# Performance work log

Measured on AMD Instinct MI355X. Metric: run time of the kernel, lower is better.

## Reference

```python
import jax, jax.numpy as jnp
import numpy as np
import math

B, S, H = 2, 2048, 2048
NH, HD, SLOTS = 16, 128, 16


def setup_inputs() -> dict:
    key = jax.random.key(0)
    k1, k2, k3, k4 = jax.random.split(key, 4)
    return {
        "hidden_states": jax.random.normal(k1, (B, S, H), dtype=jnp.float32),
        "stack": jax.random.normal(k2, (B, S, NH, SLOTS, HD), dtype=jnp.float32),
        "mask": jnp.ones((B, S, NH, SLOTS), dtype=jnp.float32),
        "W_action": jax.random.normal(k3, (3 * NH, H), dtype=jnp.float32) * 0.02,
        "b_action": jnp.zeros((3 * NH,), dtype=jnp.float32),
        "W_gate": jax.random.normal(k4, (1, HD), dtype=jnp.float32) * 0.02,
        "b_gate": jnp.zeros((1,), dtype=jnp.float32),
        "res_weight": jnp.ones((1,), dtype=jnp.float32),
    }


def reference(hidden_states, stack, mask, W_action, b_action, W_gate, b_gate, res_weight):
    b, s, h = hidden_states.shape
    nh, slots, hd = stack.shape[2], stack.shape[3], stack.shape[4]

    # action probabilities: push / pop / no-op per head
    logits = (jnp.einsum('bsh,ah->bsa', hidden_states, W_action) + b_action) / math.sqrt(hd)
    actions = jax.nn.softmax(logits.reshape(b, s, nh, 3), axis=-1)  # [B,S,NH,3]

    k_values = hidden_states.reshape(b, s, nh, hd)

    # shifted stack views (slot axis = 3)
    push_stack = jnp.concatenate([k_values[:, :, :, None, :], stack[:, :, :, :-1, :]], axis=3)
    push_mask = jnp.concatenate([jnp.ones_like(mask[:, :, :, :1]), mask[:, :, :, :-1]], axis=3)
    pop_stack = jnp.concatenate([stack[:, :, :, 1:, :], jnp.zeros_like(stack[:, :, :, :1, :])], axis=3)
    pop_mask = jnp.concatenate([mask[:, :, :, 1:], jnp.zeros_like(mask[:, :, :, :1])], axis=3)

    a_push = actions[:, :, :, 0]
    a_pop = actions[:, :, :, 1]
    a_stay = actions[:, :, :, 2]

    new_stack = (a_push[..., None, None] * push_stack
                 + a_pop[..., None, None] * pop_stack
                 + a_stay[..., None, None] * stack)  # [B,S,NH,SLOTS,HD]
    new_mask = (a_push[..., None] * push_mask
                + a_pop[..., None] * pop_mask
                + a_stay[..., None] * mask)  # [B,S,NH,SLOTS]

    # gated readout over slots
    gate_scores = jnp.einsum('bsnkd,d->bsnk', new_stack, W_gate[0]) + b_gate[0]
    gate_weights = jax.nn.softmax(gate_scores + (1.0 - new_mask) * -1e9, axis=-1)
    memory_output = jnp.einsum('bsnkd,bsnk->bsnd', new_stack, gate_weights).reshape(b, s, h)

    output = memory_output * res_weight + hidden_states
    return output, new_stack, new_mask
```

## Files before the change

kernel.cpp:

```cpp
#include <hip/hip_runtime.h>

#define Bc 2
#define Sc 2048
#define Hc 2048
#define NHc 16
#define HDc 128
#define SLOTSc 16

__global__ __launch_bounds__(512, 4) void stack_mem_fused(
    const float* __restrict__ hidden,
    const float* __restrict__ stack,
    const float* __restrict__ mask,
    const float* __restrict__ W_action,
    const float* __restrict__ b_action,
    const float* __restrict__ W_gate,
    const float* __restrict__ b_gate,
    const float* __restrict__ res_weight,
    float* __restrict__ out,
    float* __restrict__ new_stack,
    float* __restrict__ new_mask)
{
    __shared__ float hid[Hc];

    const int bs   = blockIdx.x >> 1;
    const int half = blockIdx.x & 1;
    const int tid  = threadIdx.x;
    const int lane = tid & 63;
    const int wave = tid >> 6;
    const int n    = half * 8 + wave;

    const float* hrow = hidden + (size_t)bs * Hc;
    ((float4*)hid)[tid] = ((const float4*)hrow)[tid];
    __syncthreads();

    float p0 = 0.f, p1 = 0.f, p2 = 0.f;
    {
        const float* W0 = W_action + (size_t)(3 * n) * Hc;
        const float* W1 = W0 + Hc;
        const float* W2 = W1 + Hc;
        #pragma unroll 4
        for (int i = lane; i < Hc; i += 64) {
            float hv = hid[i];
            p0 = fmaf(hv, W0[i], p0);
            p1 = fmaf(hv, W1[i], p1);
            p2 = fmaf(hv, W2[i], p2);
        }
    }
    #pragma unroll
    for (int o = 32; o; o >>= 1) {
        p0 += __shfl_xor(p0, o, 64);
        p1 += __shfl_xor(p1, o, 64);
        p2 += __shfl_xor(p2, o, 64);
    }
    const float scale = 0.08838834764831845f;
    float l0 = (p0 + b_action[3 * n + 0]) * scale;
    float l1 = (p1 + b_action[3 * n + 1]) * scale;
    float l2 = (p2 + b_action[3 * n + 2]) * scale;
    float lm = fmaxf(l0, fmaxf(l1, l2));
    float e0 = __expf(l0 - lm), e1 = __expf(l1 - lm), e2 = __expf(l2 - lm);
    float inv3 = 1.f / (e0 + e1 + e2);
    const float a_push = e0 * inv3;
    const float a_pop  = e1 * inv3;
    const float a_stay = e2 * inv3;

    const size_t sbase = ((size_t)bs * NHc + n) * (size_t)(SLOTSc * HDc);
    const float2* st2  = (const float2*)(stack + sbase);
    float2*       nst2 = (float2*)(new_stack + sbase);

    float2 kv = *(const float2*)(hid + n * HDc + 2 * lane);
    float2 wg = *(const float2*)(W_gate + 2 * lane);
    const float bg = b_gate[0];
    const float rw = res_weight[0];

    const float* mp = mask + ((size_t)bs * NHc + n) * SLOTSc;
    float m[SLOTSc];
    {
        float4 q0 = ((const float4*)mp)[0];
        float4 q1 = ((const float4*)mp)[1];
        float4 q2 = ((const float4*)mp)[2];
        float4 q3 = ((const float4*)mp)[3];
        m[0]=q0.x;  m[1]=q0.y;  m[2]=q0.z;  m[3]=q0.w;
        m[4]=q1.x;  m[5]=q1.y;  m[6]=q1.z;  m[7]=q1.w;
        m[8]=q2.x;  m[9]=q2.y;  m[10]=q2.z; m[11]=q2.w;
        m[12]=q3.x; m[13]=q3.y; m[14]=q3.z; m[15]=q3.w;
    }

    float nm[SLOTSc];
    #pragma unroll
    for (int k = 0; k < SLOTSc; ++k) {
        float pm = (k == 0) ? 1.f : m[k - 1];
        float om = (k < SLOTSc - 1) ? m[k + 1] : 0.f;
        nm[k] = a_push * pm + a_pop * om + a_stay * m[k];
    }
    {
        float msel = nm[0];
        #pragma unroll
        for (int k = 1; k < SLOTSc; ++k) if (lane == k) msel = nm[k];
        if (lane < SLOTSc)
            new_mask[((size_t)bs * NHc + n) * SLOTSc + lane] = msel;
    }
    float bias[SLOTSc];
    #pragma unroll
    for (int k = 0; k < SLOTSc; ++k)
        bias[k] = bg + (1.f - nm[k]) * -1000000000.0f;

    float2 ns[SLOTSc];
    float2 prev = kv;
    float2 cur  = st2[lane];
    #pragma unroll
    for (int k = 0; k < SLOTSc; ++k) {
        float2 nxt;
        if (k < SLOTSc - 1) nxt = st2[(k + 1) * 64 + lane];
        else { nxt.x = 0.f; nxt.y = 0.f; }
        ns[k].x = a_push * prev.x + a_pop * nxt.x + a_stay * cur.x;
        ns[k].y = a_push * prev.y + a_pop * nxt.y + a_stay * cur.y;
        nst2[k * 64 + lane] = ns[k];
        prev = cur; cur = nxt;
    }

    float gs[SLOTSc];
    #pragma unroll
    for (int k = 0; k < SLOTSc; ++k) {
        float p = ns[k].x * wg.x + ns[k].y * wg.y;
        #pragma unroll
        for (int o = 32; o; o >>= 1) p += __shfl_xor(p, o, 64);
        gs[k] = p + bias[k];
    }

    float mx = gs[0];
    #pragma unroll
    for (int k = 1; k < SLOTSc; ++k) mx = fmaxf(mx, gs[k]);
    float ssum = 0.f;
    #pragma unroll
    for (int k = 0; k < SLOTSc; ++k) { gs[k] = __expf(gs[k] - mx); ssum += gs[k]; }
    const float invs = 1.f / ssum;

    float2 mo; mo.x = 0.f; mo.y = 0.f;
    #pragma unroll
    for (int k = 0; k < SLOTSc; ++k) {
        float w = gs[k] * invs;
        mo.x = fmaf(w, ns[k].x, mo.x);
        mo.y = fmaf(w, ns[k].y, mo.y);
    }
    float2 ov;
    ov.x = mo.x * rw + kv.x;
    ov.y = mo.y * rw + kv.y;
    *(float2*)(out + (size_t)bs * Hc + n * HDc + 2 * lane) = ov;
}

extern "C" void kernel_launch(void* const* d_in, const int* in_sizes, int n_in,
                              void* d_out, int out_size, void* d_ws, size_t ws_size,
                              hipStream_t stream) {
    const float* hidden     = (const float*)d_in[0];
    const float* stack      = (const float*)d_in[1];
    const float* mask       = (const float*)d_in[2];
    const float* W_action   = (const float*)d_in[3];
    const float* b_action   = (const float*)d_in[4];
    const float* W_gate     = (const float*)d_in[5];
    const float* b_gate     = (const float*)d_in[6];
    const float* res_weight = (const float*)d_in[7];

    float* out       = (float*)d_out;
    float* new_stack = out + (size_t)Bc * Sc * Hc;
    float* new_mask  = new_stack + (size_t)Bc * Sc * NHc * SLOTSc * HDc;

    dim3 grid(Bc * Sc * 2);
    dim3 block(512);
    hipLaunchKernelGGL(stack_mem_fused, grid, block, 0, stream,
                       hidden, stack, mask, W_action, b_action,
                       W_gate, b_gate, res_weight,
                       out, new_stack, new_mask);
}
```

Baseline: 253.7 us.

## Split action-probability matvec into separate kernel and stream stack with smaller blocks

Moves the per-row action logits/softmax into a dedicated kernel writing a small workspace buffer, so the streaming stack kernel no longer recomputes the W_action dot products per head or stages hidden in shared memory. The stack kernel now uses 256-thread blocks covering 4 heads each. This removes the per-block W_action reads from the bandwidth-bound pass, at the cost of an extra launch and a workspace round trip. The actions kernel's per-thread row reads are poorly coalesced.

After: 387.6 us. +52.8%, slower.

```diff
diff --git a/kernel.cpp b/kernel.cpp
--- a/kernel.cpp
+++ b/kernel.cpp
@@ -6,13 +6,54 @@
 #define NHc 16
 #define HDc 128
 #define SLOTSc 16
+#define NROWS (Bc * Sc)
 
-__global__ __launch_bounds__(512, 4) void stack_mem_fused(
+__global__ __launch_bounds__(256) void actions_kernel(
+    const float* __restrict__ hidden,
+    const float* __restrict__ W_action,
+    const float* __restrict__ b_action,
+    float* __restrict__ actions)
+{
+    const int rl   = threadIdx.x >> 4;
+    const int head = threadIdx.x & 15;
+    const int r    = blockIdx.x * 16 + rl;
+    const int c0   = 3 * head;
+
+    const float4* A  = (const float4*)(hidden + (size_t)r * Hc);
+    const float4* B0 = (const float4*)(W_action + (size_t)c0 * Hc);
+    const float4* B1 = B0 + (Hc / 4);
+    const float4* B2 = B1 + (Hc / 4);
+
+    float s0 = 0.f, s1 = 0.f, s2 = 0.f;
+    #pragma unroll 8
+    for (int k = 0; k < Hc / 4; ++k) {
+        float4 a  = A[k];
+        float4 b0 = B0[k];
+        float4 b1 = B1[k];
+        float4 b2 = B2[k];
+        s0 = fmaf(a.x, b0.x, fmaf(a.y, b0.y, fmaf(a.z, b0.z, fmaf(a.w, b0.w, s0))));
+        s1 = fmaf(a.x, b1.x, fmaf(a.y, b1.y, fmaf(a.z, b1.z, fmaf(a.w, b1.w, s1))));
+        s2 = fmaf(a.x, b2.x, fmaf(a.y, b2.y, fmaf(a.z, b2.z, fmaf(a.w, b2.w, s2))));
+    }
+    const float scale = 0.08838834764831845f;
+    float l0 = (s0 + b_action[c0 + 0]) * scale;
+    float l1 = (s1 + b_action[c0 + 1]) * scale;
+    float l2 = (s2 + b_action[c0 + 2]) * scale;
+    float lm = fmaxf(l0, fmaxf(l1, l2));
+    float e0 = __expf(l0 - lm), e1 = __expf(l1 - lm), e2 = __expf(l2 - lm);
+    float inv = 1.f / (e0 + e1 + e2);
+
+    float* ap = actions + ((size_t)r * NHc + head) * 3;
+    ap[0] = e0 * inv;
+    ap[1] = e1 * inv;
+    ap[2] = e2 * inv;
+}
+
+__global__ __launch_bounds__(256, 4) void stack_stream(
     const float* __restrict__ hidden,
     const float* __restrict__ stack,
     const float* __restrict__ mask,
-    const float* __restrict__ W_action,
-    const float* __restrict__ b_action,
+    const float* __restrict__ actions,
     const float* __restrict__ W_gate,
     const float* __restrict__ b_gate,
     const float* __restrict__ res_weight,
@@ -20,54 +61,22 @@
     float* __restrict__ new_stack,
     float* __restrict__ new_mask)
 {
-    __shared__ float hid[Hc];
+    const int bs   = blockIdx.x >> 2;
+    const int hg   = blockIdx.x & 3;
+    const int lane = threadIdx.x & 63;
+    const int wave = threadIdx.x >> 6;
+    const int n    = hg * 4 + wave;
 
-    const int bs   = blockIdx.x >> 1;
-    const int half = blockIdx.x & 1;
-    const int tid  = threadIdx.x;
-    const int lane = tid & 63;
-    const int wave = tid >> 6;
-    const int n    = half * 8 + wave;
-
-    const float* hrow = hidden + (size_t)bs * Hc;
-    ((float4*)hid)[tid] = ((const float4*)hrow)[tid];
-    __syncthreads();
-
-    float p0 = 0.f, p1 = 0.f, p2 = 0.f;
-    {
-        const float* W0 = W_action + (size_t)(3 * n) * Hc;
-        const float* W1 = W0 + Hc;
-        const float* W2 = W1 + Hc;
-        #pragma unroll 4
-        for (int i = lane; i < Hc; i += 64) {
-            float hv = hid[i];
-            p0 = fmaf(hv, W0[i], p0);
-            p1 = fmaf(hv, W1[i], p1);
-            p2 = fmaf(hv, W2[i], p2);
-        }
-    }
-    #pragma unroll
-    for (int o = 32; o; o >>= 1) {
-        p0 += __shfl_xor(p0, o, 64);
-        p1 += __shfl_xor(p1, o, 64);
-        p2 += __shfl_xor(p2, o, 64);
-    }
-    const float scale = 0.08838834764831845f;
-    float l0 = (p0 + b_action[3 * n + 0]) * scale;
-    float l1 = (p1 + b_action[3 * n + 1]) * scale;
-    float l2 = (p2 + b_action[3 * n + 2]) * scale;
-    float lm = fmaxf(l0, fmaxf(l1, l2));
-    float e0 = __expf(l0 - lm), e1 = __expf(l1 - lm), e2 = __expf(l2 - lm);
-    float inv3 = 1.f / (e0 + e1 + e2);
-    const float a_push = e0 * inv3;
-    const float a_pop  = e1 * inv3;
-    const float a_stay = e2 * inv3;
+    const float* ap = actions + ((size_t)bs * NHc + n) * 3;
+    const float a_push = ap[0];
+    const float a_pop  = ap[1];
+    const float a_stay = ap[2];
 
     const size_t sbase = ((size_t)bs * NHc + n) * (size_t)(SLOTSc * HDc);
     const float2* st2  = (const float2*)(stack + sbase);
     float2*       nst2 = (float2*)(new_stack + sbase);
 
-    float2 kv = *(const float2*)(hid + n * HDc + 2 * lane);
+    float2 kv = *(const float2*)(hidden + (size_t)bs * Hc + n * HDc + 2 * lane);
     float2 wg = *(const float2*)(W_gate + 2 * lane);
     const float bg = b_gate[0];
     const float rw = res_weight[0];
@@ -99,10 +108,6 @@
         if (lane < SLOTSc)
             new_mask[((size_t)bs * NHc + n) * SLOTSc + lane] = msel;
     }
-    float bias[SLOTSc];
-    #pragma unroll
-    for (int k = 0; k < SLOTSc; ++k)
-        bias[k] = bg + (1.f - nm[k]) * -1000000000.0f;
 
     float2 ns[SLOTSc];
     float2 prev = kv;
@@ -124,7 +129,7 @@
         float p = ns[k].x * wg.x + ns[k].y * wg.y;
         #pragma unroll
         for (int o = 32; o; o >>= 1) p += __shfl_xor(p, o, 64);
-        gs[k] = p + bias[k];
+        gs[k] = p + bg + (1.f - nm[k]) * -1000000000.0f;
     }
 
     float mx = gs[0];
@@ -164,10 +169,12 @@
     float* new_stack = out + (size_t)Bc * Sc * Hc;
     float* new_mask  = new_stack + (size_t)Bc * Sc * NHc * SLOTSc * HDc;
 
-    dim3 grid(Bc * Sc * 2);
-    dim3 block(512);
-    hipLaunchKernelGGL(stack_mem_fused, grid, block, 0, stream,
-                       hidden, stack, mask, W_action, b_action,
-                       W_gate, b_gate, res_weight,
+    float* actions = (float*)d_ws;
+
+    hipLaunchKernelGGL(actions_kernel, dim3(NROWS / 16), dim3(256), 0, stream,
+                       hidden, W_action, b_action, actions);
+
+    hipLaunchKernelGGL(stack_stream, dim3(NROWS * 4), dim3(256), 0, stream,
+                       hidden, stack, mask, actions, W_gate, b_gate, res_weight,
                        out, new_stack, new_mask);
 }
```
